# Kernel tuning notes

Measured on AMD Instinct MI355X. Metric: run time of the kernel, lower is better.

The kernel has to match this reference:

```python
import jax, jax.numpy as jnp
import numpy as np

# VoxelGrid constants from init_kwargs
X_MIN, Y_MIN, Z_MIN = -51.2, -51.2, -3.0
X_MAX, Y_MAX, Z_MAX = 51.2, 51.2, 3.0
VOXEL = 0.5
NX = int((X_MAX - X_MIN) / VOXEL) + 1  # 205
NY = int((Y_MAX - Y_MIN) / VOXEL) + 1  # 205
NZ = int((Z_MAX - Z_MIN) / VOXEL) + 1  # 13
N_POINTS = 8_000_000


def setup_inputs() -> dict:
    key = jax.random.key(0)
    k1, k2 = jax.random.split(key)
    # points uniform inside the point cloud range
    lo = jnp.array([X_MIN, Y_MIN, Z_MIN], dtype=jnp.float32)
    hi = jnp.array([X_MAX, Y_MAX, Z_MAX], dtype=jnp.float32)
    u = jax.random.uniform(k1, (N_POINTS, 3), dtype=jnp.float32)
    points = lo + u * (hi - lo)
    # learned grid parameter, init_weights() style: N(0, 0.01)
    grid = jax.random.normal(k2, (NX, NY, NZ, 3), dtype=jnp.float32) * 0.01
    return {"points": points, "grid": grid}


def _trilinear(points, grid):
    # world -> continuous grid coords [N, 3]
    lo = jnp.array([X_MIN, Y_MIN, Z_MIN], dtype=points.dtype)
    gc = (points - lo) / jnp.asarray(VOXEL, points.dtype)

    f0 = jnp.floor(gc).astype(jnp.int32)  # [N,3]
    hi = jnp.array([NX - 1, NY - 1, NZ - 1], dtype=jnp.int32)
    i0 = jnp.clip(f0, 0, hi)        # clamped lower corner
    i1 = jnp.clip(f0 + 1, 0, hi)    # clamped upper corner

    # fractional offsets (relative to clamped lower corner, as in the torch code)
    d = gc - i0.astype(gc.dtype)    # [N,3]
    xd, yd, zd = d[:, 0:1], d[:, 1:2], d[:, 2:3]

    x0, y0, z0 = i0[:, 0], i0[:, 1], i0[:, 2]
    x1, y1, z1 = i1[:, 0], i1[:, 1], i1[:, 2]

    c000 = grid[x0, y0, z0]
    c001 = grid[x0, y0, z1]
    c010 = grid[x0, y1, z0]
    c011 = grid[x0, y1, z1]
    c100 = grid[x1, y0, z0]
    c101 = grid[x1, y0, z1]
    c110 = grid[x1, y1, z0]
    c111 = grid[x1, y1, z1]

    c00 = c000 * (1 - xd) + c100 * xd
    c01 = c001 * (1 - xd) + c101 * xd
    c10 = c010 * (1 - xd) + c110 * xd
    c11 = c011 * (1 - xd) + c111 * xd
    c0 = c00 * (1 - yd) + c10 * yd
    c1 = c01 * (1 - yd) + c11 * yd
    return c0 * (1 - zd) + c1 * zd  # [N,3] flow


def reference(points, grid):
    return _trilinear(points, grid)
```

## Files before the change

### kernel.cpp

```cpp
#include <hip/hip_runtime.h>

#define NXc 205
#define NYc 205
#define NZc 13
#define NZP 16
#define NCOL (NXc * NYc)
#define NVOXP (NCOL * NZP)
#define NGRID (NXc * NYc * NZc * 3)

typedef float        f32x4 __attribute__((ext_vector_type(4)));
typedef unsigned int u32x2 __attribute__((ext_vector_type(2)));


__global__ __launch_bounds__(256) void init_scale(unsigned int* s) {
    if (threadIdx.x == 0 && blockIdx.x == 0) s[0] = 0u;
}

__global__ __launch_bounds__(256) void grid_absmax(
    const float* __restrict__ g, unsigned int* __restrict__ smax, int n)
{
    __shared__ unsigned int red[4];
    float m = 0.0f;
    for (int i = blockIdx.x * blockDim.x + threadIdx.x; i < n; i += gridDim.x * blockDim.x)
        m = fmaxf(m, fabsf(g[i]));
#pragma unroll
    for (int off = 32; off > 0; off >>= 1)
        m = fmaxf(m, __shfl_xor(m, off));
    if ((threadIdx.x & 63) == 0) red[threadIdx.x >> 6] = __float_as_uint(m);
    __syncthreads();
    if (threadIdx.x == 0) {
        unsigned int b = red[0];
        b = max(b, red[1]); b = max(b, red[2]); b = max(b, red[3]);
        atomicMax(smax, b);
    }
}

__global__ __launch_bounds__(256) void quant_grid(
    const float* __restrict__ g, const unsigned int* __restrict__ smax,
    unsigned int* __restrict__ q)
{
    int i = blockIdx.x * blockDim.x + threadIdx.x;
    if (i >= NVOXP) return;
    int zp = i & (NZP - 1);
    int xy = i >> 4;
    unsigned int w = 512u | (512u << 10) | (512u << 20);
    if (zp < NZc) {
        float s = __uint_as_float(*smax);
        float inv = s > 0.0f ? 511.0f / s : 0.0f;
        int base = (xy * NZc + zp) * 3;
        int q0 = (int)rintf(g[base + 0] * inv);
        int q1 = (int)rintf(g[base + 1] * inv);
        int q2 = (int)rintf(g[base + 2] * inv);
        q0 = min(max(q0, -511), 511);
        q1 = min(max(q1, -511), 511);
        q2 = min(max(q2, -511), 511);
        w = (unsigned int)(q0 + 512) | ((unsigned int)(q1 + 512) << 10)
          | ((unsigned int)(q2 + 512) << 20);
    }
    q[i] = w;
}

__device__ __forceinline__ void trilerp_q10(
    float px, float py, float pz, const unsigned int* __restrict__ q, float sdec,
    float& r0, float& r1, float& r2)
{
    float gx = (px + 51.2f) * 2.0f;
    float gy = (py + 51.2f) * 2.0f;
    float gz = (pz + 3.0f) * 2.0f;
    int fx = (int)floorf(gx), fy = (int)floorf(gy), fz = (int)floorf(gz);
    int x0 = min(max(fx, 0), NXc - 1);
    int y0 = min(max(fy, 0), NYc - 1);
    int z0 = min(max(fz, 0), NZc - 1);
    int x1 = min(max(fx + 1, 0), NXc - 1);
    int y1 = min(max(fy + 1, 0), NYc - 1);
    float xd = gx - (float)x0, yd = gy - (float)y0, zd = gz - (float)z0;

    int i00 = ((x0 * NYc + y0) << 4) + z0;
    int i01 = ((x0 * NYc + y1) << 4) + z0;
    int i10 = ((x1 * NYc + y0) << 4) + z0;
    int i11 = ((x1 * NYc + y1) << 4) + z0;

    u32x2 a = *(const u32x2*)(q + i00);
    u32x2 b = *(const u32x2*)(q + i01);
    u32x2 c = *(const u32x2*)(q + i10);
    u32x2 d = *(const u32x2*)(q + i11);

    float zs = 1.0f - zd;
    float v00x = (float)(a.x & 1023u) * zs + (float)(a.y & 1023u) * zd;
    float v00y = (float)((a.x >> 10) & 1023u) * zs + (float)((a.y >> 10) & 1023u) * zd;
    float v00z = (float)((a.x >> 20) & 1023u) * zs + (float)((a.y >> 20) & 1023u) * zd;

    float v01x = (float)(b.x & 1023u) * zs + (float)(b.y & 1023u) * zd;
    float v01y = (float)((b.x >> 10) & 1023u) * zs + (float)((b.y >> 10) & 1023u) * zd;
    float v01z = (float)((b.x >> 20) & 1023u) * zs + (float)((b.y >> 20) & 1023u) * zd;

    float v10x = (float)(c.x & 1023u) * zs + (float)(c.y & 1023u) * zd;
    float v10y = (float)((c.x >> 10) & 1023u) * zs + (float)((c.y >> 10) & 1023u) * zd;
    float v10z = (float)((c.x >> 20) & 1023u) * zs + (float)((c.y >> 20) & 1023u) * zd;

    float v11x = (float)(d.x & 1023u) * zs + (float)(d.y & 1023u) * zd;
    float v11y = (float)((d.x >> 10) & 1023u) * zs + (float)((d.y >> 10) & 1023u) * zd;
    float v11z = (float)((d.x >> 20) & 1023u) * zs + (float)((d.y >> 20) & 1023u) * zd;

    float xs = 1.0f - xd, ys = 1.0f - yd;
    float p0x = v00x * xs + v10x * xd, p1x = v01x * xs + v11x * xd;
    float p0y = v00y * xs + v10y * xd, p1y = v01y * xs + v11y * xd;
    float p0z = v00z * xs + v10z * xd, p1z = v01z * xs + v11z * xd;
    float bx = p0x * ys + p1x * yd;
    float by = p0y * ys + p1y * yd;
    float bz = p0z * ys + p1z * yd;
    r0 = (bx - 512.0f) * sdec;
    r1 = (by - 512.0f) * sdec;
    r2 = (bz - 512.0f) * sdec;
}

__global__ __launch_bounds__(256) void trilerp_quad_q10_kernel(
    const f32x4* __restrict__ pts4, const unsigned int* __restrict__ q,
    const unsigned int* __restrict__ smax, f32x4* __restrict__ out4, int nquad)
{
    int j = blockIdx.x * blockDim.x + threadIdx.x;
    if (j >= nquad) return;
    float sdec = __uint_as_float(*smax) * (1.0f / 511.0f);
    f32x4 A = __builtin_nontemporal_load(&pts4[3 * j + 0]);
    f32x4 B = __builtin_nontemporal_load(&pts4[3 * j + 1]);
    f32x4 C = __builtin_nontemporal_load(&pts4[3 * j + 2]);
    float px[4] = {A.x, A.w, B.z, C.y};
    float py[4] = {A.y, B.x, B.w, C.z};
    float pz[4] = {A.z, B.y, C.x, C.w};
    float o[12];
#pragma unroll
    for (int k = 0; k < 4; ++k) {
        trilerp_q10(px[k], py[k], pz[k], q, sdec, o[3 * k + 0], o[3 * k + 1], o[3 * k + 2]);
    }
    f32x4 O0 = {o[0], o[1], o[2],  o[3]};
    f32x4 O1 = {o[4], o[5], o[6],  o[7]};
    f32x4 O2 = {o[8], o[9], o[10], o[11]};
    __builtin_nontemporal_store(O0, &out4[3 * j + 0]);
    __builtin_nontemporal_store(O1, &out4[3 * j + 1]);
    __builtin_nontemporal_store(O2, &out4[3 * j + 2]);
}

__global__ __launch_bounds__(64) void trilerp_tail_q10_kernel(
    const float* __restrict__ pts, const unsigned int* __restrict__ q,
    const unsigned int* __restrict__ smax, float* __restrict__ out, int start, int n)
{
    int i = start + blockIdx.x * blockDim.x + threadIdx.x;
    if (i >= n) return;
    float sdec = __uint_as_float(*smax) * (1.0f / 511.0f);
    float r0, r1, r2;
    trilerp_q10(pts[3 * i], pts[3 * i + 1], pts[3 * i + 2], q, sdec, r0, r1, r2);
    out[3 * i + 0] = r0;
    out[3 * i + 1] = r1;
    out[3 * i + 2] = r2;
}

__global__ __launch_bounds__(256) void trilerp_raw_kernel(
    const float* __restrict__ pts, const float* __restrict__ g,
    float* __restrict__ out, int n)
{
    int i = blockIdx.x * blockDim.x + threadIdx.x;
    if (i >= n) return;
    float gx = (pts[3 * i + 0] + 51.2f) * 2.0f;
    float gy = (pts[3 * i + 1] + 51.2f) * 2.0f;
    float gz = (pts[3 * i + 2] + 3.0f) * 2.0f;
    int fx = (int)floorf(gx), fy = (int)floorf(gy), fz = (int)floorf(gz);
    int x0 = min(max(fx, 0), NXc - 1);
    int y0 = min(max(fy, 0), NYc - 1);
    int z0 = min(max(fz, 0), NZc - 1);
    int x1 = min(max(fx + 1, 0), NXc - 1);
    int y1 = min(max(fy + 1, 0), NYc - 1);
    int z1 = min(max(fz + 1, 0), NZc - 1);
    float xd = gx - (float)x0, yd = gy - (float)y0, zd = gz - (float)z0;
    const float* p000 = g + ((x0 * NYc + y0) * NZc + z0) * 3;
    const float* p001 = g + ((x0 * NYc + y0) * NZc + z1) * 3;
    const float* p010 = g + ((x0 * NYc + y1) * NZc + z0) * 3;
    const float* p011 = g + ((x0 * NYc + y1) * NZc + z1) * 3;
    const float* p100 = g + ((x1 * NYc + y0) * NZc + z0) * 3;
    const float* p101 = g + ((x1 * NYc + y0) * NZc + z1) * 3;
    const float* p110 = g + ((x1 * NYc + y1) * NZc + z0) * 3;
    const float* p111 = g + ((x1 * NYc + y1) * NZc + z1) * 3;
    float xs = 1.0f - xd, ys = 1.0f - yd, zs = 1.0f - zd;
#pragma unroll
    for (int c = 0; c < 3; ++c) {
        float c00 = p000[c] * xs + p100[c] * xd;
        float c01 = p001[c] * xs + p101[c] * xd;
        float c10 = p010[c] * xs + p110[c] * xd;
        float c11 = p011[c] * xs + p111[c] * xd;
        float c0 = c00 * ys + c10 * yd;
        float c1 = c01 * ys + c11 * yd;
        out[3 * i + c] = c0 * zs + c1 * zd;
    }
}

extern "C" void kernel_launch(void* const* d_in, const int* in_sizes, int n_in,
                              void* d_out, int out_size, void* d_ws, size_t ws_size,
                              hipStream_t stream) {
    const float* pts  = (const float*)d_in[0];
    const float* grid = (const float*)d_in[1];
    float* out = (float*)d_out;
    int n = in_sizes[0] / 3;

    size_t need = 256 + (size_t)NVOXP * 4;
    if (ws_size >= need) {
        unsigned int* smax = (unsigned int*)d_ws;
        unsigned int* q = (unsigned int*)((char*)d_ws + 256);
        init_scale<<<1, 256, 0, stream>>>(smax);
        grid_absmax<<<512, 256, 0, stream>>>(grid, smax, NGRID);
        quant_grid<<<(NVOXP + 255) / 256, 256, 0, stream>>>(grid, smax, q);
        int nquad = n / 4;
        if (nquad > 0) {
            trilerp_quad_q10_kernel<<<(nquad + 255) / 256, 256, 0, stream>>>(
                (const f32x4*)pts, q, smax, (f32x4*)out, nquad);
        }
        int done = nquad * 4;
        if (done < n) {
            int rem = n - done;
            trilerp_tail_q10_kernel<<<(rem + 63) / 64, 64, 0, stream>>>(
                pts, q, smax, out, done, n);
        }
    } else {
        trilerp_raw_kernel<<<(n + 255) / 256, 256, 0, stream>>>(pts, grid, out, n);
    }
}
```

Measured before the change: 304.8 us.

## Store x-neighbor pairs per cell so each trilerp needs two 16-byte loads

The quantized grid now stores, for each (x,y,z) cell, the packed 10-bit value of that cell and of its x+1 neighbor side by side in an 8-byte entry, without z padding. A single 16-byte load then fetches all four x/z corners for one y row, so each point needs two gathers instead of four 8-byte gathers. The cost is a larger quantized grid from duplicated x data. There is also a reliance on 8-byte-aligned 16-byte loads and on reading past the z column when z0 is at the last plane, where the result is weighted by zd.

```diff
diff --git a/kernel.cpp b/kernel.cpp
--- a/kernel.cpp
+++ b/kernel.cpp
@@ -3,13 +3,11 @@
 #define NXc 205
 #define NYc 205
 #define NZc 13
-#define NZP 16
-#define NCOL (NXc * NYc)
-#define NVOXP (NCOL * NZP)
+#define NCELL (NXc * NYc * NZc)
 #define NGRID (NXc * NYc * NZc * 3)
 
 typedef float        f32x4 __attribute__((ext_vector_type(4)));
-typedef unsigned int u32x2 __attribute__((ext_vector_type(2)));
+typedef unsigned int u32x4 __attribute__((ext_vector_type(4)));
 
 
 __global__ __launch_bounds__(256) void init_scale(unsigned int* s) {
@@ -35,33 +33,34 @@
     }
 }
 
-__global__ __launch_bounds__(256) void quant_grid(
+__device__ __forceinline__ unsigned int enc3(const float* v, float inv) {
+    int q0 = min(max((int)rintf(v[0] * inv), -511), 511);
+    int q1 = min(max((int)rintf(v[1] * inv), -511), 511);
+    int q2 = min(max((int)rintf(v[2] * inv), -511), 511);
+    return (unsigned int)(q0 + 512) | ((unsigned int)(q1 + 512) << 10)
+         | ((unsigned int)(q2 + 512) << 20);
+}
+
+__global__ __launch_bounds__(256) void quant_grid_xpair(
     const float* __restrict__ g, const unsigned int* __restrict__ smax,
-    unsigned int* __restrict__ q)
+    uint2* __restrict__ q)
 {
     int i = blockIdx.x * blockDim.x + threadIdx.x;
-    if (i >= NVOXP) return;
-    int zp = i & (NZP - 1);
-    int xy = i >> 4;
-    unsigned int w = 512u | (512u << 10) | (512u << 20);
-    if (zp < NZc) {
-        float s = __uint_as_float(*smax);
-        float inv = s > 0.0f ? 511.0f / s : 0.0f;
-        int base = (xy * NZc + zp) * 3;
-        int q0 = (int)rintf(g[base + 0] * inv);
-        int q1 = (int)rintf(g[base + 1] * inv);
-        int q2 = (int)rintf(g[base + 2] * inv);
-        q0 = min(max(q0, -511), 511);
-        q1 = min(max(q1, -511), 511);
-        q2 = min(max(q2, -511), 511);
-        w = (unsigned int)(q0 + 512) | ((unsigned int)(q1 + 512) << 10)
-          | ((unsigned int)(q2 + 512) << 20);
-    }
-    q[i] = w;
-}
-
-__device__ __forceinline__ void trilerp_q10(
-    float px, float py, float pz, const unsigned int* __restrict__ q, float sdec,
+    if (i >= NCELL) return;
+    int z = i % NZc;
+    int xy = i / NZc;
+    int y = xy % NYc;
+    int x = xy / NYc;
+    int x1 = min(x + 1, NXc - 1);
+    float s = __uint_as_float(*smax);
+    float inv = s > 0.0f ? 511.0f / s : 0.0f;
+    const float* v0 = g + ((x  * NYc + y) * NZc + z) * 3;
+    const float* v1 = g + ((x1 * NYc + y) * NZc + z) * 3;
+    q[i] = make_uint2(enc3(v0, inv), enc3(v1, inv));
+}
+
+__device__ __forceinline__ void trilerp_xp(
+    float px, float py, float pz, const char* __restrict__ qb, float sdec,
     float& r0, float& r1, float& r2)
 {
     float gx = (px + 51.2f) * 2.0f;
@@ -71,51 +70,39 @@
     int x0 = min(max(fx, 0), NXc - 1);
     int y0 = min(max(fy, 0), NYc - 1);
     int z0 = min(max(fz, 0), NZc - 1);
-    int x1 = min(max(fx + 1, 0), NXc - 1);
     int y1 = min(max(fy + 1, 0), NYc - 1);
     float xd = gx - (float)x0, yd = gy - (float)y0, zd = gz - (float)z0;
 
-    int i00 = ((x0 * NYc + y0) << 4) + z0;
-    int i01 = ((x0 * NYc + y1) << 4) + z0;
-    int i10 = ((x1 * NYc + y0) << 4) + z0;
-    int i11 = ((x1 * NYc + y1) << 4) + z0;
-
-    u32x2 a = *(const u32x2*)(q + i00);
-    u32x2 b = *(const u32x2*)(q + i01);
-    u32x2 c = *(const u32x2*)(q + i10);
-    u32x2 d = *(const u32x2*)(q + i11);
-
-    float zs = 1.0f - zd;
-    float v00x = (float)(a.x & 1023u) * zs + (float)(a.y & 1023u) * zd;
-    float v00y = (float)((a.x >> 10) & 1023u) * zs + (float)((a.y >> 10) & 1023u) * zd;
-    float v00z = (float)((a.x >> 20) & 1023u) * zs + (float)((a.y >> 20) & 1023u) * zd;
-
-    float v01x = (float)(b.x & 1023u) * zs + (float)(b.y & 1023u) * zd;
-    float v01y = (float)((b.x >> 10) & 1023u) * zs + (float)((b.y >> 10) & 1023u) * zd;
-    float v01z = (float)((b.x >> 20) & 1023u) * zs + (float)((b.y >> 20) & 1023u) * zd;
-
-    float v10x = (float)(c.x & 1023u) * zs + (float)(c.y & 1023u) * zd;
-    float v10y = (float)((c.x >> 10) & 1023u) * zs + (float)((c.y >> 10) & 1023u) * zd;
-    float v10z = (float)((c.x >> 20) & 1023u) * zs + (float)((c.y >> 20) & 1023u) * zd;
-
-    float v11x = (float)(d.x & 1023u) * zs + (float)(d.y & 1023u) * zd;
-    float v11y = (float)((d.x >> 10) & 1023u) * zs + (float)((d.y >> 10) & 1023u) * zd;
-    float v11z = (float)((d.x >> 20) & 1023u) * zs + (float)((d.y >> 20) & 1023u) * zd;
-
-    float xs = 1.0f - xd, ys = 1.0f - yd;
-    float p0x = v00x * xs + v10x * xd, p1x = v01x * xs + v11x * xd;
-    float p0y = v00y * xs + v10y * xd, p1y = v01y * xs + v11y * xd;
-    float p0z = v00z * xs + v10z * xd, p1z = v01z * xs + v11z * xd;
-    float bx = p0x * ys + p1x * yd;
-    float by = p0y * ys + p1y * yd;
-    float bz = p0z * ys + p1z * yd;
-    r0 = (bx - 512.0f) * sdec;
-    r1 = (by - 512.0f) * sdec;
-    r2 = (bz - 512.0f) * sdec;
-}
-
-__global__ __launch_bounds__(256) void trilerp_quad_q10_kernel(
-    const f32x4* __restrict__ pts4, const unsigned int* __restrict__ q,
+    int iA = ((x0 * NYc + y0) * NZc + z0) * 8;
+    int iB = ((x0 * NYc + y1) * NZc + z0) * 8;
+    u32x4 A = *(const u32x4*)(qb + iA);
+    u32x4 B = *(const u32x4*)(qb + iB);
+
+    float zs = 1.0f - zd, xs = 1.0f - xd, ys = 1.0f - yd;
+#define COMPO(sh, out) { \
+    float a00 = (float)((A.x >> sh) & 1023u); \
+    float a10 = (float)((A.y >> sh) & 1023u); \
+    float a01 = (float)((A.z >> sh) & 1023u); \
+    float a11 = (float)((A.w >> sh) & 1023u); \
+    float b00 = (float)((B.x >> sh) & 1023u); \
+    float b10 = (float)((B.y >> sh) & 1023u); \
+    float b01 = (float)((B.z >> sh) & 1023u); \
+    float b11 = (float)((B.w >> sh) & 1023u); \
+    float va0 = a00 * zs + a01 * zd; \
+    float va1 = a10 * zs + a11 * zd; \
+    float vb0 = b00 * zs + b01 * zd; \
+    float vb1 = b10 * zs + b11 * zd; \
+    float pa = va0 * xs + va1 * xd; \
+    float pb = vb0 * xs + vb1 * xd; \
+    out = ((pa * ys + pb * yd) - 512.0f) * sdec; }
+    COMPO(0,  r0);
+    COMPO(10, r1);
+    COMPO(20, r2);
+#undef COMPO
+}
+
+__global__ __launch_bounds__(256) void trilerp_quad_xp_kernel(
+    const f32x4* __restrict__ pts4, const char* __restrict__ qb,
     const unsigned int* __restrict__ smax, f32x4* __restrict__ out4, int nquad)
 {
     int j = blockIdx.x * blockDim.x + threadIdx.x;
@@ -130,7 +117,7 @@
     float o[12];
 #pragma unroll
     for (int k = 0; k < 4; ++k) {
-        trilerp_q10(px[k], py[k], pz[k], q, sdec, o[3 * k + 0], o[3 * k + 1], o[3 * k + 2]);
+        trilerp_xp(px[k], py[k], pz[k], qb, sdec, o[3 * k + 0], o[3 * k + 1], o[3 * k + 2]);
     }
     f32x4 O0 = {o[0], o[1], o[2],  o[3]};
     f32x4 O1 = {o[4], o[5], o[6],  o[7]};
@@ -140,15 +127,15 @@
     __builtin_nontemporal_store(O2, &out4[3 * j + 2]);
 }
 
-__global__ __launch_bounds__(64) void trilerp_tail_q10_kernel(
-    const float* __restrict__ pts, const unsigned int* __restrict__ q,
+__global__ __launch_bounds__(64) void trilerp_tail_xp_kernel(
+    const float* __restrict__ pts, const char* __restrict__ qb,
     const unsigned int* __restrict__ smax, float* __restrict__ out, int start, int n)
 {
     int i = start + blockIdx.x * blockDim.x + threadIdx.x;
     if (i >= n) return;
     float sdec = __uint_as_float(*smax) * (1.0f / 511.0f);
     float r0, r1, r2;
-    trilerp_q10(pts[3 * i], pts[3 * i + 1], pts[3 * i + 2], q, sdec, r0, r1, r2);
+    trilerp_xp(pts[3 * i], pts[3 * i + 1], pts[3 * i + 2], qb, sdec, r0, r1, r2);
     out[3 * i + 0] = r0;
     out[3 * i + 1] = r1;
     out[3 * i + 2] = r2;
@@ -200,23 +187,23 @@
     float* out = (float*)d_out;
     int n = in_sizes[0] / 3;
 
-    size_t need = 256 + (size_t)NVOXP * 4;
+    size_t need = 256 + (size_t)NCELL * 8 + 16;
     if (ws_size >= need) {
         unsigned int* smax = (unsigned int*)d_ws;
-        unsigned int* q = (unsigned int*)((char*)d_ws + 256);
+        uint2* q = (uint2*)((char*)d_ws + 256);
         init_scale<<<1, 256, 0, stream>>>(smax);
         grid_absmax<<<512, 256, 0, stream>>>(grid, smax, NGRID);
-        quant_grid<<<(NVOXP + 255) / 256, 256, 0, stream>>>(grid, smax, q);
+        quant_grid_xpair<<<(NCELL + 255) / 256, 256, 0, stream>>>(grid, smax, q);
         int nquad = n / 4;
         if (nquad > 0) {
-            trilerp_quad_q10_kernel<<<(nquad + 255) / 256, 256, 0, stream>>>(
-                (const f32x4*)pts, q, smax, (f32x4*)out, nquad);
+            trilerp_quad_xp_kernel<<<(nquad + 255) / 256, 256, 0, stream>>>(
+                (const f32x4*)pts, (const char*)q, smax, (f32x4*)out, nquad);
         }
         int done = nquad * 4;
         if (done < n) {
             int rem = n - done;
-            trilerp_tail_q10_kernel<<<(rem + 63) / 64, 64, 0, stream>>>(
-                pts, q, smax, out, done, n);
+            trilerp_tail_xp_kernel<<<(rem + 63) / 64, 64, 0, stream>>>(
+                pts, (const char*)q, smax, out, done, n);
         }
     } else {
         trilerp_raw_kernel<<<(n + 255) / 256, 256, 0, stream>>>(pts, grid, out, n);
```

Measured after the change: 283.1 us. 1.08x faster.
